# Performance work log

Measured on AMD Instinct MI355X. Metric: run time of the kernel, lower is better.

Reference implementation:

```python
import jax, jax.numpy as jnp
import numpy as np

NUM_BOXES = 200
BATCH = 256
LEVEL_HW = [(200, 334), (100, 167), (50, 84), (25, 42)]
IM_X, IM_Y = 1333, 800


def setup_inputs() -> dict:
    key = jax.random.key(0)
    ks = jax.random.split(key, 8)
    inp = {}
    for i, (h, w) in enumerate(LEVEL_HW):
        inp[f"h_masks_{i}"] = jax.random.uniform(ks[i], (BATCH, 1, h, w), dtype=jnp.float32)
    # xyxy boxes in image coords: x1,y1 uniform, x2=x1+width, y2=y1+height
    x1 = jax.random.uniform(ks[4], (NUM_BOXES,), minval=0.0, maxval=IM_X * 0.6)
    y1 = jax.random.uniform(ks[5], (NUM_BOXES,), minval=0.0, maxval=IM_Y * 0.6)
    bw = jax.random.uniform(ks[6], (NUM_BOXES,), minval=10.0, maxval=IM_X * 0.3)
    bh = jax.random.uniform(ks[7], (NUM_BOXES,), minval=10.0, maxval=IM_Y * 0.3)
    inp["label"] = jnp.stack([x1, y1, x1 + bw, y1 + bh], axis=1).astype(jnp.float32)
    inp["im_dimx"] = IM_X
    inp["im_dimy"] = IM_Y
    return inp


def _level_loss(hi, boxes, im_dimx, im_dimy):
    b, _, h, w = hi.shape
    sx = w / im_dimx
    sy = h / im_dimy
    # round-half-to-even (matches torch .round()), then clamp as in original
    x1 = jnp.clip(jnp.round(boxes[:, 0] * sx), 0, w - 1).astype(jnp.int32)  # [N]
    y1 = jnp.clip(jnp.round(boxes[:, 1] * sy), 0, h - 1).astype(jnp.int32)
    x2 = jnp.clip(jnp.round(boxes[:, 2] * sx), 0, w).astype(jnp.int32)
    y2 = jnp.clip(jnp.round(boxes[:, 3] * sy), 0, h).astype(jnp.int32)
    # original skip condition (box contributes nothing if any holds)
    valid = (x2 > x1) & (y2 > y1) & (x1 + x2 < w) & (y1 + y2 < h)  # [N]
    xs = jnp.arange(w)
    ys = jnp.arange(h)
    in_x = (xs[None, :] >= x1[:, None]) & (xs[None, :] < x2[:, None])  # [N,w]
    in_y = (ys[None, :] >= y1[:, None]) & (ys[None, :] < y2[:, None])  # [N,h]
    # union rasterization over boxes onto a single [h,w] grid
    mask = jnp.any(valid[:, None, None] & in_y[:, :, None] & in_x[:, None, :], axis=0)
    tn_pixel = float(b * h * w)
    pi = jnp.sum(mask.astype(hi.dtype)) / tn_pixel
    return (jnp.sum(hi) / tn_pixel - pi) ** 2


def reference(h_masks_0, h_masks_1, h_masks_2, h_masks_3, label, im_dimx, im_dimy):
    levels = [h_masks_0, h_masks_1, h_masks_2, h_masks_3]
    losses = [_level_loss(hi, label, im_dimx, im_dimy) for hi in levels]
    return sum(losses) / len(losses)
```

## Files before the change

kernel.cpp:

```cpp
#include <hip/hip_runtime.h>


__device__ __forceinline__ double wave_red_d(double v) {
#pragma unroll
  for (int off = 32; off > 0; off >>= 1) v += __shfl_down(v, off, 64);
  return v;
}
__device__ __forceinline__ int wave_red_i(int v) {
#pragma unroll
  for (int off = 32; off > 0; off >>= 1) v += __shfl_down(v, off, 64);
  return v;
}

#define SUM_BLOCKS 1024
#define RAST_BLOCKS 12
#define COUNTS_OFF 32768

__global__ __launch_bounds__(256) void sum_levels_kernel(
    const float4* __restrict__ p0, const float4* __restrict__ p1,
    const float4* __restrict__ p2, const float4* __restrict__ p3,
    int n0, int n1, int n2, int n3, double* __restrict__ partials) {
  const int gid = blockIdx.x * blockDim.x + threadIdx.x;
  const int stride = gridDim.x * blockDim.x;
  double a0 = 0.0, a1 = 0.0, a2 = 0.0, a3 = 0.0;
  for (int i = gid; i < n0; i += stride) {
    float4 v = p0[i];
    a0 += (double)((v.x + v.y) + (v.z + v.w));
  }
  for (int i = gid; i < n1; i += stride) {
    float4 v = p1[i];
    a1 += (double)((v.x + v.y) + (v.z + v.w));
  }
  for (int i = gid; i < n2; i += stride) {
    float4 v = p2[i];
    a2 += (double)((v.x + v.y) + (v.z + v.w));
  }
  for (int i = gid; i < n3; i += stride) {
    float4 v = p3[i];
    a3 += (double)((v.x + v.y) + (v.z + v.w));
  }
  a0 = wave_red_d(a0); a1 = wave_red_d(a1); a2 = wave_red_d(a2); a3 = wave_red_d(a3);
  __shared__ double sh[4][4];
  const int wid = threadIdx.x >> 6;
  if ((threadIdx.x & 63) == 0) {
    sh[wid][0] = a0; sh[wid][1] = a1; sh[wid][2] = a2; sh[wid][3] = a3;
  }
  __syncthreads();
  if (threadIdx.x == 0) {
    double* dst = &partials[blockIdx.x * 4];
#pragma unroll
    for (int l = 0; l < 4; l++) dst[l] = sh[0][l] + sh[1][l] + sh[2][l] + sh[3][l];
  }
}

__global__ __launch_bounds__(256) void raster_kernel(
    const float* __restrict__ label, int nboxes,
    const int* __restrict__ dimx_p, const int* __restrict__ dimy_p,
    int* __restrict__ counts) {
  __shared__ int sx1[4][256], sx2[4][256], sy1[4][256], sy2[4][256];
  const int tid = threadIdx.x;
  const double imx = (double)dimx_p[0];
  const double imy = (double)dimy_p[0];
  const int nb = nboxes < 256 ? nboxes : 256;

  for (int idx = tid; idx < 4 * nb; idx += 256) {
    const int lvl = idx / nb;
    const int j = idx - lvl * nb;
    const int w = (lvl == 0) ? 334 : (lvl == 1) ? 167 : (lvl == 2) ? 84 : 42;
    const int h = (lvl == 0) ? 200 : (lvl == 1) ? 100 : (lvl == 2) ? 50 : 25;
    const float sx = (float)((double)w / imx);
    const float sy = (float)((double)h / imy);
    float b0 = label[j * 4 + 0], b1 = label[j * 4 + 1];
    float b2 = label[j * 4 + 2], b3 = label[j * 4 + 3];
    int x1 = (int)fminf(fmaxf(rintf(b0 * sx), 0.0f), (float)(w - 1));
    int y1 = (int)fminf(fmaxf(rintf(b1 * sy), 0.0f), (float)(h - 1));
    int x2 = (int)fminf(fmaxf(rintf(b2 * sx), 0.0f), (float)w);
    int y2 = (int)fminf(fmaxf(rintf(b3 * sy), 0.0f), (float)h);
    bool valid = (x2 > x1) && (y2 > y1) && (x1 + x2 < w) && (y1 + y2 < h);
    sx1[lvl][j] = x1; sx2[lvl][j] = x2;
    sy1[lvl][j] = valid ? y1 : 0x7fffffff;
    sy2[lvl][j] = y2;
  }
  __syncthreads();

  int c0 = 0, c1 = 0, c2 = 0, c3 = 0;
  for (int t = blockIdx.x * 256 + tid; t < 3000; t += gridDim.x * 256) {
    int lvl, r, wd;
    if (t < 2200)      { lvl = 0; unsigned u = t;        r = u / 11; wd = u - r * 11; }
    else if (t < 2800) { lvl = 1; unsigned u = t - 2200; r = u / 6;  wd = u - r * 6; }
    else if (t < 2950) { lvl = 2; unsigned u = t - 2800; r = u / 3;  wd = u - r * 3; }
    else               { lvl = 3; unsigned u = t - 2950; r = u >> 1; wd = u & 1; }
    const int col0 = wd << 5;
    unsigned m = 0;
    for (int j = 0; j < nb; j++) {
      const int y1 = sy1[lvl][j], y2 = sy2[lvl][j];
      const int a = sx1[lvl][j], b = sx2[lvl][j];
      const bool inrow = (r >= y1) & (r < y2);
      int lo = a - col0; lo = lo > 0 ? lo : 0;
      int hi = b - col0; hi = hi < 32 ? hi : 32;
      if (inrow && hi > lo) {
        unsigned mh = (hi >= 32) ? 0xffffffffu : ((1u << (hi & 31)) - 1u);
        m |= mh & (0xffffffffu << (lo & 31));
      }
    }
    const int pc = __popc(m);
    if (lvl == 0) c0 += pc; else if (lvl == 1) c1 += pc;
    else if (lvl == 2) c2 += pc; else c3 += pc;
  }
  c0 = wave_red_i(c0); c1 = wave_red_i(c1); c2 = wave_red_i(c2); c3 = wave_red_i(c3);
  __shared__ int shc[4][4];
  const int wid = tid >> 6;
  if ((tid & 63) == 0) { shc[wid][0] = c0; shc[wid][1] = c1; shc[wid][2] = c2; shc[wid][3] = c3; }
  __syncthreads();
  if (tid == 0) {
    int* dst = &counts[blockIdx.x * 4];
#pragma unroll
    for (int l = 0; l < 4; l++) dst[l] = shc[0][l] + shc[1][l] + shc[2][l] + shc[3][l];
  }
}

__global__ __launch_bounds__(256) void finish_kernel(
    const double* __restrict__ partials, const int* __restrict__ counts,
    float* __restrict__ out) {
  const int tid = threadIdx.x;
  double s0 = 0.0, s1 = 0.0, s2 = 0.0, s3 = 0.0;
  for (int b = tid; b < SUM_BLOCKS; b += 256) {
    s0 += partials[b * 4 + 0]; s1 += partials[b * 4 + 1];
    s2 += partials[b * 4 + 2]; s3 += partials[b * 4 + 3];
  }
  int c0 = 0, c1 = 0, c2 = 0, c3 = 0;
  if (tid < RAST_BLOCKS) {
    c0 = counts[tid * 4 + 0]; c1 = counts[tid * 4 + 1];
    c2 = counts[tid * 4 + 2]; c3 = counts[tid * 4 + 3];
  }
  s0 = wave_red_d(s0); s1 = wave_red_d(s1); s2 = wave_red_d(s2); s3 = wave_red_d(s3);
  c0 = wave_red_i(c0); c1 = wave_red_i(c1); c2 = wave_red_i(c2); c3 = wave_red_i(c3);
  __shared__ double shd[4][4];
  __shared__ int shi[4][4];
  const int wid = tid >> 6;
  if ((tid & 63) == 0) {
    shd[wid][0] = s0; shd[wid][1] = s1; shd[wid][2] = s2; shd[wid][3] = s3;
    shi[wid][0] = c0; shi[wid][1] = c1; shi[wid][2] = c2; shi[wid][3] = c3;
  }
  __syncthreads();
  if (tid == 0) {
    const double HH[4] = {200.0, 100.0, 50.0, 25.0};
    const double WW[4] = {334.0, 167.0, 84.0, 42.0};
    double loss = 0.0;
#pragma unroll
    for (int l = 0; l < 4; l++) {
      double s = shd[0][l] + shd[1][l] + shd[2][l] + shd[3][l];
      double c = (double)(shi[0][l] + shi[1][l] + shi[2][l] + shi[3][l]);
      double tn = 256.0 * HH[l] * WW[l];
      double d = (s - c) / tn;
      loss += d * d;
    }
    out[0] = (float)(loss * 0.25);
  }
}

extern "C" void kernel_launch(void* const* d_in, const int* in_sizes, int n_in,
                              void* d_out, int out_size, void* d_ws, size_t ws_size,
                              hipStream_t stream) {
  const float4* p0 = (const float4*)d_in[0];
  const float4* p1 = (const float4*)d_in[1];
  const float4* p2 = (const float4*)d_in[2];
  const float4* p3 = (const float4*)d_in[3];
  const float* label = (const float*)d_in[4];
  const int* dimx = (const int*)d_in[5];
  const int* dimy = (const int*)d_in[6];
  float* out = (float*)d_out;
  double* partials = (double*)d_ws;
  int* counts = (int*)((char*)d_ws + COUNTS_OFF);

  const int n0 = in_sizes[0] / 4;
  const int n1 = in_sizes[1] / 4;
  const int n2 = in_sizes[2] / 4;
  const int n3 = in_sizes[3] / 4;
  const int nboxes = in_sizes[4] / 4;

  sum_levels_kernel<<<SUM_BLOCKS, 256, 0, stream>>>(p0, p1, p2, p3, n0, n1, n2, n3, partials);
  raster_kernel<<<RAST_BLOCKS, 256, 0, stream>>>(label, nboxes, dimx, dimy, counts);
  finish_kernel<<<1, 256, 0, stream>>>(partials, counts, out);
}
```

Baseline: 133.1 us.

## Fuse sum, raster and finish kernels into one launch with last-block reduction

Merges the three kernels into a single launch. The first 12 blocks rasterize the box union and the rest sum the mask levels, and an atomic counter selects the last finishing block to do the final reduction. This removes two kernel launches and lets rasterization overlap the bandwidth-bound summation. It also unrolls the level-0 and level-1 load loops with extra accumulators to keep more loads in flight, at the cost of an added memset, threadfences and an atomic per block.

```diff
diff --git a/kernel.cpp b/kernel.cpp
--- a/kernel.cpp
+++ b/kernel.cpp
@@ -1,5 +1,11 @@
 #include <hip/hip_runtime.h>
 
+
+#define NBLK 1024
+#define RAST_BLOCKS 12
+#define SUM_BLOCKS (NBLK - RAST_BLOCKS)
+#define PART_OFF 64
+#define CNT_OFF (64 + NBLK * 4 * 8)
 
 __device__ __forceinline__ double wave_red_d(double v) {
 #pragma unroll
@@ -12,119 +18,138 @@
   return v;
 }
 
-#define SUM_BLOCKS 1024
-#define RAST_BLOCKS 12
-#define COUNTS_OFF 32768
-
-__global__ __launch_bounds__(256) void sum_levels_kernel(
+__global__ __launch_bounds__(256) void fused_loss_kernel(
     const float4* __restrict__ p0, const float4* __restrict__ p1,
     const float4* __restrict__ p2, const float4* __restrict__ p3,
-    int n0, int n1, int n2, int n3, double* __restrict__ partials) {
-  const int gid = blockIdx.x * blockDim.x + threadIdx.x;
-  const int stride = gridDim.x * blockDim.x;
-  double a0 = 0.0, a1 = 0.0, a2 = 0.0, a3 = 0.0;
-  for (int i = gid; i < n0; i += stride) {
-    float4 v = p0[i];
-    a0 += (double)((v.x + v.y) + (v.z + v.w));
-  }
-  for (int i = gid; i < n1; i += stride) {
-    float4 v = p1[i];
-    a1 += (double)((v.x + v.y) + (v.z + v.w));
-  }
-  for (int i = gid; i < n2; i += stride) {
-    float4 v = p2[i];
-    a2 += (double)((v.x + v.y) + (v.z + v.w));
-  }
-  for (int i = gid; i < n3; i += stride) {
-    float4 v = p3[i];
-    a3 += (double)((v.x + v.y) + (v.z + v.w));
-  }
-  a0 = wave_red_d(a0); a1 = wave_red_d(a1); a2 = wave_red_d(a2); a3 = wave_red_d(a3);
-  __shared__ double sh[4][4];
-  const int wid = threadIdx.x >> 6;
-  if ((threadIdx.x & 63) == 0) {
-    sh[wid][0] = a0; sh[wid][1] = a1; sh[wid][2] = a2; sh[wid][3] = a3;
-  }
-  __syncthreads();
-  if (threadIdx.x == 0) {
-    double* dst = &partials[blockIdx.x * 4];
-#pragma unroll
-    for (int l = 0; l < 4; l++) dst[l] = sh[0][l] + sh[1][l] + sh[2][l] + sh[3][l];
-  }
-}
-
-__global__ __launch_bounds__(256) void raster_kernel(
+    int n0, int n1, int n2, int n3,
     const float* __restrict__ label, int nboxes,
     const int* __restrict__ dimx_p, const int* __restrict__ dimy_p,
-    int* __restrict__ counts) {
-  __shared__ int sx1[4][256], sx2[4][256], sy1[4][256], sy2[4][256];
+    unsigned* __restrict__ ws_ctr, float* __restrict__ out) {
+  double* partials = (double*)((char*)ws_ctr + PART_OFF);
+  int* counts = (int*)((char*)ws_ctr + CNT_OFF);
   const int tid = threadIdx.x;
-  const double imx = (double)dimx_p[0];
-  const double imy = (double)dimy_p[0];
-  const int nb = nboxes < 256 ? nboxes : 256;
-
-  for (int idx = tid; idx < 4 * nb; idx += 256) {
-    const int lvl = idx / nb;
-    const int j = idx - lvl * nb;
-    const int w = (lvl == 0) ? 334 : (lvl == 1) ? 167 : (lvl == 2) ? 84 : 42;
-    const int h = (lvl == 0) ? 200 : (lvl == 1) ? 100 : (lvl == 2) ? 50 : 25;
-    const float sx = (float)((double)w / imx);
-    const float sy = (float)((double)h / imy);
-    float b0 = label[j * 4 + 0], b1 = label[j * 4 + 1];
-    float b2 = label[j * 4 + 2], b3 = label[j * 4 + 3];
-    int x1 = (int)fminf(fmaxf(rintf(b0 * sx), 0.0f), (float)(w - 1));
-    int y1 = (int)fminf(fmaxf(rintf(b1 * sy), 0.0f), (float)(h - 1));
-    int x2 = (int)fminf(fmaxf(rintf(b2 * sx), 0.0f), (float)w);
-    int y2 = (int)fminf(fmaxf(rintf(b3 * sy), 0.0f), (float)h);
-    bool valid = (x2 > x1) && (y2 > y1) && (x1 + x2 < w) && (y1 + y2 < h);
-    sx1[lvl][j] = x1; sx2[lvl][j] = x2;
-    sy1[lvl][j] = valid ? y1 : 0x7fffffff;
-    sy2[lvl][j] = y2;
-  }
-  __syncthreads();
-
-  int c0 = 0, c1 = 0, c2 = 0, c3 = 0;
-  for (int t = blockIdx.x * 256 + tid; t < 3000; t += gridDim.x * 256) {
-    int lvl, r, wd;
-    if (t < 2200)      { lvl = 0; unsigned u = t;        r = u / 11; wd = u - r * 11; }
-    else if (t < 2800) { lvl = 1; unsigned u = t - 2200; r = u / 6;  wd = u - r * 6; }
-    else if (t < 2950) { lvl = 2; unsigned u = t - 2800; r = u / 3;  wd = u - r * 3; }
-    else               { lvl = 3; unsigned u = t - 2950; r = u >> 1; wd = u & 1; }
+  const int blk = blockIdx.x;
+
+  __shared__ double shd[4][4];
+  __shared__ int shi[4][4];
+  __shared__ bool s_last;
+
+  if (blk < RAST_BLOCKS) {
+    __shared__ int sx1[4][256], sx2[4][256], sy1[4][256], sy2[4][256];
+    const double imx = (double)dimx_p[0];
+    const double imy = (double)dimy_p[0];
+    const int nb = nboxes < 256 ? nboxes : 256;
+    for (int idx = tid; idx < 4 * nb; idx += 256) {
+      const int lvl = idx / nb;
+      const int j = idx - lvl * nb;
+      const int w = (lvl == 0) ? 334 : (lvl == 1) ? 167 : (lvl == 2) ? 84 : 42;
+      const int h = (lvl == 0) ? 200 : (lvl == 1) ? 100 : (lvl == 2) ? 50 : 25;
+      const float sx = (float)((double)w / imx);
+      const float sy = (float)((double)h / imy);
+      float b0 = label[j * 4 + 0], b1 = label[j * 4 + 1];
+      float b2 = label[j * 4 + 2], b3 = label[j * 4 + 3];
+      int x1 = (int)fminf(fmaxf(rintf(b0 * sx), 0.0f), (float)(w - 1));
+      int y1 = (int)fminf(fmaxf(rintf(b1 * sy), 0.0f), (float)(h - 1));
+      int x2 = (int)fminf(fmaxf(rintf(b2 * sx), 0.0f), (float)w);
+      int y2 = (int)fminf(fmaxf(rintf(b3 * sy), 0.0f), (float)h);
+      bool valid = (x2 > x1) && (y2 > y1) && (x1 + x2 < w) && (y1 + y2 < h);
+      sx1[lvl][j] = x1; sx2[lvl][j] = x2;
+      sy1[lvl][j] = valid ? y1 : 0x7fffffff;
+      sy2[lvl][j] = y2;
+    }
+    __syncthreads();
+    const int t = blk * 256 + tid;
+    int lvl = 0, r = 0, wd = 0;
+    bool has = (t < 3000);
+    if (has) {
+      if (t < 2200)      { lvl = 0; unsigned u = t;        r = u / 11; wd = u - r * 11; }
+      else if (t < 2800) { lvl = 1; unsigned u = t - 2200; r = u / 6;  wd = u - r * 6; }
+      else if (t < 2950) { lvl = 2; unsigned u = t - 2800; r = u / 3;  wd = u - r * 3; }
+      else               { lvl = 3; unsigned u = t - 2950; r = u >> 1; wd = u & 1; }
+    }
     const int col0 = wd << 5;
     unsigned m = 0;
-    for (int j = 0; j < nb; j++) {
-      const int y1 = sy1[lvl][j], y2 = sy2[lvl][j];
-      const int a = sx1[lvl][j], b = sx2[lvl][j];
-      const bool inrow = (r >= y1) & (r < y2);
-      int lo = a - col0; lo = lo > 0 ? lo : 0;
-      int hi = b - col0; hi = hi < 32 ? hi : 32;
-      if (inrow && hi > lo) {
-        unsigned mh = (hi >= 32) ? 0xffffffffu : ((1u << (hi & 31)) - 1u);
-        m |= mh & (0xffffffffu << (lo & 31));
+    if (has) {
+      for (int j = 0; j < nb; j++) {
+        const int y1 = sy1[lvl][j], y2 = sy2[lvl][j];
+        const int a = sx1[lvl][j], b = sx2[lvl][j];
+        const bool inrow = (r >= y1) & (r < y2);
+        int lo = a - col0; lo = lo > 0 ? lo : 0;
+        int hi = b - col0; hi = hi < 32 ? hi : 32;
+        if (inrow && hi > lo) {
+          unsigned mh = (hi >= 32) ? 0xffffffffu : ((1u << (hi & 31)) - 1u);
+          m |= mh & (0xffffffffu << (lo & 31));
+        }
       }
     }
     const int pc = __popc(m);
-    if (lvl == 0) c0 += pc; else if (lvl == 1) c1 += pc;
-    else if (lvl == 2) c2 += pc; else c3 += pc;
-  }
-  c0 = wave_red_i(c0); c1 = wave_red_i(c1); c2 = wave_red_i(c2); c3 = wave_red_i(c3);
-  __shared__ int shc[4][4];
-  const int wid = tid >> 6;
-  if ((tid & 63) == 0) { shc[wid][0] = c0; shc[wid][1] = c1; shc[wid][2] = c2; shc[wid][3] = c3; }
+    int c0 = (lvl == 0) ? pc : 0, c1 = (lvl == 1) ? pc : 0;
+    int c2 = (lvl == 2) ? pc : 0, c3 = (lvl == 3) ? pc : 0;
+    c0 = wave_red_i(c0); c1 = wave_red_i(c1); c2 = wave_red_i(c2); c3 = wave_red_i(c3);
+    const int wid = tid >> 6;
+    if ((tid & 63) == 0) { shi[wid][0] = c0; shi[wid][1] = c1; shi[wid][2] = c2; shi[wid][3] = c3; }
+    __syncthreads();
+    if (tid == 0) {
+      int* dst = &counts[blk * 4];
+#pragma unroll
+      for (int l = 0; l < 4; l++) dst[l] = shi[0][l] + shi[1][l] + shi[2][l] + shi[3][l];
+    }
+  } else {
+    const int gid = (blk - RAST_BLOCKS) * 256 + tid;
+    const int stride = SUM_BLOCKS * 256;
+    double a0 = 0.0, a0b = 0.0, a1 = 0.0, a1b = 0.0, a2 = 0.0, a3 = 0.0;
+    int i = gid;
+    for (; i + 3 * stride < n0; i += 4 * stride) {
+      float4 v0 = p0[i], v1 = p0[i + stride], v2 = p0[i + 2 * stride], v3 = p0[i + 3 * stride];
+      a0  += (double)((v0.x + v0.y) + (v0.z + v0.w)) + (double)((v1.x + v1.y) + (v1.z + v1.w));
+      a0b += (double)((v2.x + v2.y) + (v2.z + v2.w)) + (double)((v3.x + v3.y) + (v3.z + v3.w));
+    }
+    for (; i < n0; i += stride) {
+      float4 v = p0[i];
+      a0 += (double)((v.x + v.y) + (v.z + v.w));
+    }
+    a0 += a0b;
+    i = gid;
+    for (; i + stride < n1; i += 2 * stride) {
+      float4 v0 = p1[i], v1 = p1[i + stride];
+      a1  += (double)((v0.x + v0.y) + (v0.z + v0.w));
+      a1b += (double)((v1.x + v1.y) + (v1.z + v1.w));
+    }
+    for (; i < n1; i += stride) {
+      float4 v = p1[i];
+      a1 += (double)((v.x + v.y) + (v.z + v.w));
+    }
+    a1 += a1b;
+    for (i = gid; i < n2; i += stride) {
+      float4 v = p2[i];
+      a2 += (double)((v.x + v.y) + (v.z + v.w));
+    }
+    for (i = gid; i < n3; i += stride) {
+      float4 v = p3[i];
+      a3 += (double)((v.x + v.y) + (v.z + v.w));
+    }
+    a0 = wave_red_d(a0); a1 = wave_red_d(a1); a2 = wave_red_d(a2); a3 = wave_red_d(a3);
+    const int wid = tid >> 6;
+    if ((tid & 63) == 0) { shd[wid][0] = a0; shd[wid][1] = a1; shd[wid][2] = a2; shd[wid][3] = a3; }
+    __syncthreads();
+    if (tid == 0) {
+      double* dst = &partials[blk * 4];
+#pragma unroll
+      for (int l = 0; l < 4; l++) dst[l] = shd[0][l] + shd[1][l] + shd[2][l] + shd[3][l];
+    }
+  }
+
+  __threadfence();
+  if (tid == 0) {
+    unsigned old = atomicAdd(ws_ctr, 1u);
+    s_last = (old == NBLK - 1);
+  }
   __syncthreads();
-  if (tid == 0) {
-    int* dst = &counts[blockIdx.x * 4];
-#pragma unroll
-    for (int l = 0; l < 4; l++) dst[l] = shc[0][l] + shc[1][l] + shc[2][l] + shc[3][l];
-  }
-}
-
-__global__ __launch_bounds__(256) void finish_kernel(
-    const double* __restrict__ partials, const int* __restrict__ counts,
-    float* __restrict__ out) {
-  const int tid = threadIdx.x;
+  if (!s_last) return;
+  __threadfence();
+
   double s0 = 0.0, s1 = 0.0, s2 = 0.0, s3 = 0.0;
-  for (int b = tid; b < SUM_BLOCKS; b += 256) {
+  for (int b = RAST_BLOCKS + tid; b < NBLK; b += 256) {
     s0 += partials[b * 4 + 0]; s1 += partials[b * 4 + 1];
     s2 += partials[b * 4 + 2]; s3 += partials[b * 4 + 3];
   }
@@ -135,8 +160,7 @@
   }
   s0 = wave_red_d(s0); s1 = wave_red_d(s1); s2 = wave_red_d(s2); s3 = wave_red_d(s3);
   c0 = wave_red_i(c0); c1 = wave_red_i(c1); c2 = wave_red_i(c2); c3 = wave_red_i(c3);
-  __shared__ double shd[4][4];
-  __shared__ int shi[4][4];
+  __syncthreads();
   const int wid = tid >> 6;
   if ((tid & 63) == 0) {
     shd[wid][0] = s0; shd[wid][1] = s1; shd[wid][2] = s2; shd[wid][3] = s3;
@@ -169,9 +193,6 @@
   const float* label = (const float*)d_in[4];
   const int* dimx = (const int*)d_in[5];
   const int* dimy = (const int*)d_in[6];
-  float* out = (float*)d_out;
-  double* partials = (double*)d_ws;
-  int* counts = (int*)((char*)d_ws + COUNTS_OFF);
 
   const int n0 = in_sizes[0] / 4;
   const int n1 = in_sizes[1] / 4;
@@ -179,7 +200,8 @@
   const int n3 = in_sizes[3] / 4;
   const int nboxes = in_sizes[4] / 4;
 
-  sum_levels_kernel<<<SUM_BLOCKS, 256, 0, stream>>>(p0, p1, p2, p3, n0, n1, n2, n3, partials);
-  raster_kernel<<<RAST_BLOCKS, 256, 0, stream>>>(label, nboxes, dimx, dimy, counts);
-  finish_kernel<<<1, 256, 0, stream>>>(partials, counts, out);
-}
+  hipMemsetAsync(d_ws, 0, 64, stream);
+  fused_loss_kernel<<<NBLK, 256, 0, stream>>>(
+      p0, p1, p2, p3, n0, n1, n2, n3, label, nboxes, dimx, dimy,
+      (unsigned*)d_ws, (float*)d_out);
+}
```

New measurement: 194.8 us. 1.46x slower.
